# Performance work log

Measured on AMD Instinct MI355X. Metric: run time of the kernel, lower is better.

## Reference

```python
import jax, jax.numpy as jnp
import numpy as np

DIM = 2048
DT_RANK = 64
DIM_INNER = 2048
D_STATE = 32
B_SZ = 4
L = 2048


def setup_inputs() -> dict:
    key = jax.random.key(0)
    ks = jax.random.split(key, 6)
    x = jax.random.normal(ks[0], (B_SZ, L, DIM), dtype=jnp.float32)
    z = jax.random.normal(ks[1], (B_SZ, L, DIM_INNER), dtype=jnp.float32)
    # proj_bc: Linear(dim, dt_rank + 2*d_state, bias=False)
    W_bc = jax.random.normal(ks[2], (DT_RANK + 2 * D_STATE, DIM), dtype=jnp.float32) * (DIM ** -0.5)
    # dt_proj: maps dt_rank -> dim_inner (as intended in Mamba)
    W_dt = jax.random.normal(ks[3], (DIM_INNER, DT_RANK), dtype=jnp.float32) * (DT_RANK ** -0.5)
    b_dt = jax.random.normal(ks[4], (DIM_INNER,), dtype=jnp.float32) * 0.1
    # A = arange(1, d_state+1) repeated per channel; A_log = log(A)
    A_log = jnp.log(jnp.tile(jnp.arange(1, D_STATE + 1, dtype=jnp.float32), (DIM_INNER, 1)))
    D_param = jnp.ones((DIM_INNER,), dtype=jnp.float32)
    return {"x": x, "z": z, "W_bc": W_bc, "W_dt": W_dt, "b_dt": b_dt, "A_log": A_log, "D_param": D_param}


def _selective_scan(u, delta, A, Bm, Cm, D_param):
    # u, delta: [b, l, d]; Bm, Cm: [b, l, n]; A: [d, n]; D_param: [d]
    def step(h, inp):
        delta_t, B_t, C_t, u_t = inp  # [b,d], [b,n], [b,n], [b,d]
        dA = jnp.exp(delta_t[:, :, None] * A[None])          # [b, d, n]
        dBu = (delta_t * u_t)[:, :, None] * B_t[:, None, :]  # [b, d, n]
        h = dA * h + dBu
        y_t = jnp.einsum('bdn,bn->bd', h, C_t)
        return h, y_t

    b = u.shape[0]
    h0 = jnp.zeros((b, A.shape[0], A.shape[1]), dtype=u.dtype)
    xs = (jnp.moveaxis(delta, 1, 0), jnp.moveaxis(Bm, 1, 0),
          jnp.moveaxis(Cm, 1, 0), jnp.moveaxis(u, 1, 0))
    _, ys = jax.lax.scan(step, h0, xs)          # ys: [l, b, d]
    y = jnp.moveaxis(ys, 0, 1)                  # [b, l, d]
    return y + u * D_param[None, None, :]


def reference(x, z, W_bc, W_dt, b_dt, A_log, D_param):
    A = -jnp.exp(A_log)                                      # [d, n]
    deltaBC = jnp.einsum('bld,od->blo', x, W_bc)             # [b, l, r+2n]
    dt_r = deltaBC[..., :DT_RANK]
    Bm = deltaBC[..., DT_RANK:DT_RANK + D_STATE]             # [b, l, n]
    Cm = deltaBC[..., DT_RANK + D_STATE:]                    # [b, l, n]
    dt = jnp.einsum('blr,dr->bld', dt_r, W_dt)               # [b, l, d]
    delta = jax.nn.softplus(dt + b_dt[None, None, :])        # delta_softplus + delta_bias
    y = _selective_scan(x, delta, A, Bm, Cm, D_param)        # [b, l, d]
    return y
```

## Files before the change

kernel.cpp:

```cpp
#include <hip/hip_runtime.h>

#define L_SEQ 2048
#define NDIM 2048
#define DINNER 2048
#define NSTATE 32
#define BSZ 4
#define DTR 64
#define NROWS (BSZ * L_SEQ)
#define TCH 32

typedef short bf16x8 __attribute__((ext_vector_type(8)));
typedef float f32x4 __attribute__((ext_vector_type(4)));
typedef unsigned int uint_t;

#if __has_builtin(__builtin_amdgcn_exp2f)
#define EXP2(v) __builtin_amdgcn_exp2f(v)
#else
#define EXP2(v) exp2f(v)
#endif
#define LOG2E 1.44269504f

__device__ __forceinline__ uint_t bf1(float a) {
  uint_t u = __float_as_uint(a);
  return (u + 0x7FFFu + ((u >> 16) & 1u)) >> 16;
}
__device__ __forceinline__ uint_t pkbf(float a, float b) {
  return bf1(a) | (bf1(b) << 16);
}

#define WBC_ELEMS (128 * NDIM)
#define WDT_ELEMS (DINNER * DTR)
__global__ __launch_bounds__(256) void k_conv(const float* __restrict__ Wbc,
                                              const float* __restrict__ Wdt,
                                              unsigned short* __restrict__ o) {
  const int i = blockIdx.x * 256 + threadIdx.x;
  if (i < WBC_ELEMS)
    o[i] = (unsigned short)bf1(Wbc[i]);
  else
    o[i] = (unsigned short)bf1(Wdt[i - WBC_ELEMS]);
}

__global__ __launch_bounds__(512) void k_dbc_mfma(const float* __restrict__ x,
                                                  const unsigned short* __restrict__ Wb,
                                                  float* __restrict__ dbc) {
  __shared__ unsigned short xl[32][72];
  __shared__ unsigned short wl[128][72];
  const int tid = threadIdx.x;
  const int wave = tid >> 6, lane = tid & 63;
  const int row0 = blockIdx.x * 32;
  const int wrow0 = (wave & 1) * 16;
  const int wcol0 = (wave >> 1) * 32;
  const int fr = lane & 15, fk = (lane >> 4) * 8;

  f32x4 acc[2];
#pragma unroll
  for (int i = 0; i < 2; ++i) acc[i] = (f32x4)(0.f);

  const int xr = tid >> 4, xk = (tid & 15) * 4;
  const int wc = tid & 127, wh = (tid >> 7) * 16;

  for (int kb = 0; kb < NDIM; kb += 64) {
    const float4 xa = *(const float4*)(x + (size_t)(row0 + xr) * NDIM + kb + xk);
    uint4 wv0 = *(const uint4*)(Wb + (size_t)wc * NDIM + kb + wh);
    uint4 wv1 = *(const uint4*)(Wb + (size_t)wc * NDIM + kb + wh + 8);
    __syncthreads();
    uint2 xp = {pkbf(xa.x, xa.y), pkbf(xa.z, xa.w)};
    *(uint2*)&xl[xr][xk] = xp;
    *(uint4*)&wl[wc][wh] = wv0;
    *(uint4*)&wl[wc][wh + 8] = wv1;
    __syncthreads();
#pragma unroll
    for (int ks = 0; ks < 2; ++ks) {
      const bf16x8 af = *(const bf16x8*)&xl[wrow0 + fr][ks * 32 + fk];
#pragma unroll
      for (int nt = 0; nt < 2; ++nt) {
        const bf16x8 bfv = *(const bf16x8*)&wl[wcol0 + nt * 16 + fr][ks * 32 + fk];
        acc[nt] = __builtin_amdgcn_mfma_f32_16x16x32_bf16(af, bfv, acc[nt], 0, 0, 0);
      }
    }
  }
#pragma unroll
  for (int nt = 0; nt < 2; ++nt)
#pragma unroll
    for (int reg = 0; reg < 4; ++reg)
      dbc[(size_t)(row0 + wrow0 + (lane >> 4) * 4 + reg) * 128 + wcol0 + nt * 16 + fr] =
          acc[nt][reg];
}

__global__ __launch_bounds__(256) void k_dt_mfma(const float* __restrict__ dbc,
                                                 const unsigned short* __restrict__ Wd,
                                                 const float* __restrict__ bdt,
                                                 float* __restrict__ dy) {
  __shared__ unsigned short al[32][72];
  const int tid = threadIdx.x;
  const int wave = tid >> 6, lane = tid & 63;
  const int row0 = blockIdx.y * 32;
  const int c0 = blockIdx.x * 256;
  const int wrow0 = (wave & 1) * 16;
  const int wc0 = c0 + (wave >> 1) * 128;
  const int fr = lane & 15, fk = (lane >> 4) * 8;

  {
    const int ar = tid >> 3, ak = (tid & 7) * 8;
    const float4 pa = *(const float4*)(dbc + (size_t)(row0 + ar) * 128 + ak);
    const float4 pb = *(const float4*)(dbc + (size_t)(row0 + ar) * 128 + ak + 4);
    uint4 ap = {pkbf(pa.x, pa.y), pkbf(pa.z, pa.w), pkbf(pb.x, pb.y), pkbf(pb.z, pb.w)};
    *(uint4*)&al[ar][ak] = ap;
  }
  __syncthreads();

  f32x4 acc[8];
#pragma unroll
  for (int i = 0; i < 8; ++i) acc[i] = (f32x4)(0.f);

#pragma unroll
  for (int ks = 0; ks < 2; ++ks) {
    const bf16x8 af = *(const bf16x8*)&al[wrow0 + fr][ks * 32 + fk];
#pragma unroll
    for (int nt = 0; nt < 8; ++nt) {
      const int col = wc0 + nt * 16 + fr;
      const bf16x8 bfv = *(const bf16x8*)(Wd + (size_t)col * 64 + ks * 32 + fk);
      acc[nt] = __builtin_amdgcn_mfma_f32_16x16x32_bf16(af, bfv, acc[nt], 0, 0, 0);
    }
  }

#pragma unroll
  for (int nt = 0; nt < 8; ++nt) {
    const int col = wc0 + nt * 16 + fr;
    const float bias = bdt[col];
#pragma unroll
    for (int reg = 0; reg < 4; ++reg) {
      const float v = acc[nt][reg] + bias;
      const float sp = (v > 20.f) ? v : __logf(1.f + __expf(v));
      dy[(size_t)(row0 + wrow0 + (lane >> 4) * 4 + reg) * DINNER + col] = sp;
    }
  }
}

__global__ __launch_bounds__(256) void k_dbc(const float* __restrict__ x,
                                             const float* __restrict__ Wbc,
                                             float* __restrict__ dbc) {
  __shared__ float xs[32][36];
  __shared__ float ws[32][132];
  const int tid = threadIdx.x;
  const int tx = tid & 31;
  const int ty = tid >> 5;
  const int row0 = blockIdx.x * 32;
  float acc[4][4];
#pragma unroll
  for (int i = 0; i < 4; ++i)
#pragma unroll
    for (int j = 0; j < 4; ++j) acc[i][j] = 0.f;
  for (int kb = 0; kb < NDIM; kb += 32) {
    {
      const int r = tid >> 3;
      const int k0 = (tid & 7) * 4;
      const float4 v = *(const float4*)(x + (size_t)(row0 + r) * NDIM + kb + k0);
      *(float4*)&xs[r][k0] = v;
    }
    {
      const int col = tid & 127;
      const int k0 = (tid >> 7) * 16;
#pragma unroll
      for (int j = 0; j < 4; ++j) {
        const float4 v = *(const float4*)(Wbc + (size_t)col * NDIM + kb + k0 + j * 4);
        ws[k0 + j * 4 + 0][col] = v.x;
        ws[k0 + j * 4 + 1][col] = v.y;
        ws[k0 + j * 4 + 2][col] = v.z;
        ws[k0 + j * 4 + 3][col] = v.w;
      }
    }
    __syncthreads();
#pragma unroll
    for (int k = 0; k < 32; k += 4) {
      float a_[4][4];
#pragma unroll
      for (int i = 0; i < 4; ++i) {
        const float4 av = *(const float4*)&xs[ty * 4 + i][k];
        a_[i][0] = av.x; a_[i][1] = av.y; a_[i][2] = av.z; a_[i][3] = av.w;
      }
#pragma unroll
      for (int kk = 0; kk < 4; ++kk) {
        const float4 bv = *(const float4*)&ws[k + kk][tx * 4];
        float b_[4] = {bv.x, bv.y, bv.z, bv.w};
#pragma unroll
        for (int i = 0; i < 4; ++i)
#pragma unroll
          for (int j = 0; j < 4; ++j)
            acc[i][j] = fmaf(a_[i][kk], b_[j], acc[i][j]);
      }
    }
    __syncthreads();
  }
#pragma unroll
  for (int i = 0; i < 4; ++i) {
    float4 o = {acc[i][0], acc[i][1], acc[i][2], acc[i][3]};
    *(float4*)(dbc + (size_t)(row0 + ty * 4 + i) * 128 + tx * 4) = o;
  }
}

__global__ __launch_bounds__(256) void k_dt(const float* __restrict__ dbc,
                                            const float* __restrict__ Wdt,
                                            const float* __restrict__ bdt,
                                            float* dy) {
  __shared__ float asn[16][68];
  __shared__ float wst[64][132];
  const int tid = threadIdx.x;
  const int tx = tid & 31;
  const int ty = tid >> 5;
  const int row0 = blockIdx.y * 16;
  const int col0 = blockIdx.x * 128;
  {
    const int r = tid >> 4;
    const int k0 = (tid & 15) * 4;
    const float4 v = *(const float4*)(dbc + (size_t)(row0 + r) * 128 + k0);
    *(float4*)&asn[r][k0] = v;
  }
  {
    const int col = tid & 127;
    const int k0 = (tid >> 7) * 32;
#pragma unroll
    for (int j = 0; j < 8; ++j) {
      const float4 v = *(const float4*)(Wdt + (size_t)(col0 + col) * 64 + k0 + j * 4);
      wst[k0 + j * 4 + 0][col] = v.x;
      wst[k0 + j * 4 + 1][col] = v.y;
      wst[k0 + j * 4 + 2][col] = v.z;
      wst[k0 + j * 4 + 3][col] = v.w;
    }
  }
  __syncthreads();
  float acc[2][4];
#pragma unroll
  for (int i = 0; i < 2; ++i)
#pragma unroll
    for (int j = 0; j < 4; ++j) acc[i][j] = 0.f;
#pragma unroll
  for (int k = 0; k < 64; k += 4) {
    float a_[2][4];
#pragma unroll
    for (int i = 0; i < 2; ++i) {
      const float4 av = *(const float4*)&asn[ty * 2 + i][k];
      a_[i][0] = av.x; a_[i][1] = av.y; a_[i][2] = av.z; a_[i][3] = av.w;
    }
#pragma unroll
    for (int kk = 0; kk < 4; ++kk) {
      const float4 bv = *(const float4*)&wst[k + kk][tx * 4];
      float b_[4] = {bv.x, bv.y, bv.z, bv.w};
#pragma unroll
      for (int i = 0; i < 2; ++i)
#pragma unroll
        for (int j = 0; j < 4; ++j)
          acc[i][j] = fmaf(a_[i][kk], b_[j], acc[i][j]);
    }
  }
  const int c = col0 + tx * 4;
  const float4 bb = *(const float4*)(bdt + c);
  const float bias[4] = {bb.x, bb.y, bb.z, bb.w};
#pragma unroll
  for (int i = 0; i < 2; ++i) {
    float o[4];
#pragma unroll
    for (int j = 0; j < 4; ++j) {
      const float v = acc[i][j] + bias[j];
      o[j] = (v > 20.f) ? v : __logf(1.f + __expf(v));
    }
    float4 ov = {o[0], o[1], o[2], o[3]};
    *(float4*)(dy + (size_t)(row0 + ty * 2 + i) * DINNER + c) = ov;
  }
}

template <int CTRL>
__device__ __forceinline__ float dpp_mov(float v) {
  return __int_as_float(
      __builtin_amdgcn_update_dpp(0, __float_as_int(v), CTRL, 0xF, 0xF, true));
}
__device__ __forceinline__ float red16(float p) {
  p += dpp_mov<0xB1>(p);
  p += dpp_mov<0x4E>(p);
  p += dpp_mov<0x141>(p);
  p += dpp_mov<0x140>(p);
  return p;
}
__device__ __forceinline__ float xor16_add(float p) {
#if __has_builtin(__builtin_amdgcn_permlane16_swap)
  typedef unsigned u2v __attribute__((ext_vector_type(2)));
  u2v s = __builtin_amdgcn_permlane16_swap(__float_as_uint(p),
                                           __float_as_uint(p), false, false);
  return __uint_as_float(s.x) + __uint_as_float(s.y);
#else
  return p + __int_as_float(
                 __builtin_amdgcn_ds_swizzle(__float_as_int(p), 0x401F));
#endif
}

__global__ __launch_bounds__(512) void k_scan512(const float* __restrict__ x,
                                                 const float* __restrict__ dbc,
                                                 const float* __restrict__ Alog,
                                                 const float* __restrict__ Dpar,
                                                 float* __restrict__ dy) {
  __shared__ float sDU[2][16][68];
  __shared__ float sBC[2][16][128];
  __shared__ float sY[2][32][17];

  const int tid = threadIdx.x;
  const int nn = tid & 31, ch = tid >> 5;
  const int dd = tid & 15, tl = tid >> 4;
  const int dg = blockIdx.x & 127;
  const int b = blockIdx.x >> 7;
  const int d0 = dg * 16;
  const int NCHK = L_SEQ / TCH;

  const float An2 = -__expf(Alog[(size_t)(d0 + ch) * NSTATE + nn]) * LOG2E;
  const float Dd = Dpar[d0 + dd];
  const size_t segbase = (size_t)b * L_SEQ;

  float u_cur;
  {
    const size_t rX = (segbase + tl) * DINNER + d0 + dd;
    const float dv = dy[rX];
    const float uv = x[rX];
    *(float2*)&sDU[0][dd][(tl >> 1) * 4 + (tl & 1) * 2] = make_float2(dv, dv * uv);
    u_cur = uv;
    const size_t rB = (segbase + ch) * 128 + 64 + nn;
    *(float2*)&sBC[0][ch >> 1][nn * 4 + (ch & 1) * 2] =
        make_float2(dbc[rB], dbc[rB + 32]);
    *(float2*)&sBC[0][(ch >> 1) + 8][nn * 4 + (ch & 1) * 2] =
        make_float2(dbc[rB + 16 * 128], dbc[rB + 16 * 128 + 32]);
  }
  __syncthreads();

  float h = 0.f;
  for (int c = 0; c < NCHK; ++c) {
    const int cb = c & 1;
    float dnx = 0.f, unx = 0.f;
    float2 bc0 = make_float2(0.f, 0.f), bc1 = make_float2(0.f, 0.f);
    if (c < NCHK - 1) {
      const size_t rX = (segbase + (c + 1) * TCH + tl) * DINNER + d0 + dd;
      dnx = dy[rX];
      unx = x[rX];
      const size_t rB = (segbase + (c + 1) * TCH + ch) * 128 + 64 + nn;
      bc0 = make_float2(dbc[rB], dbc[rB + 32]);
      bc1 = make_float2(dbc[rB + 16 * 128], dbc[rB + 16 * 128 + 32]);
    }

    const float* pDU = &sDU[cb][ch][0];
    const float* pBC = &sBC[cb][0][nn * 4];
    float yv = 0.f;
#pragma unroll
    for (int t2 = 0; t2 < TCH / 2; ++t2) {
      const float4 du = *(const float4*)(pDU + t2 * 4);
      const float4 bc = *(const float4*)(pBC + t2 * 128);
      {
        const float dA = EXP2(du.x * An2);
        h = fmaf(dA, h, du.y * bc.x);
        const float yy = xor16_add(red16(h * bc.y));
        yv = (nn == 2 * t2) ? yy : yv;
      }
      {
        const float dA = EXP2(du.z * An2);
        h = fmaf(dA, h, du.w * bc.z);
        const float yy = xor16_add(red16(h * bc.w));
        yv = (nn == 2 * t2 + 1) ? yy : yv;
      }
    }
    sY[cb][nn][ch] = yv;

    if (c < NCHK - 1) {
      *(float2*)&sDU[cb ^ 1][dd][(tl >> 1) * 4 + (tl & 1) * 2] =
          make_float2(dnx, dnx * unx);
      *(float2*)&sBC[cb ^ 1][ch >> 1][nn * 4 + (ch & 1) * 2] = bc0;
      *(float2*)&sBC[cb ^ 1][(ch >> 1) + 8][nn * 4 + (ch & 1) * 2] = bc1;
    }
    __syncthreads();

    dy[(segbase + c * TCH + tl) * DINNER + d0 + dd] =
        fmaf(u_cur, Dd, sY[cb][tl][dd]);
    u_cur = unx;
  }
}

extern "C" void kernel_launch(void* const* d_in, const int* in_sizes, int n_in,
                              void* d_out, int out_size, void* d_ws, size_t ws_size,
                              hipStream_t stream) {
  const float* x    = (const float*)d_in[0];
  const float* Wbc  = (const float*)d_in[2];
  const float* Wdt  = (const float*)d_in[3];
  const float* bdt  = (const float*)d_in[4];
  const float* Alog = (const float*)d_in[5];
  const float* Dpar = (const float*)d_in[6];
  float* dy  = (float*)d_out;
  float* dbc = (float*)d_ws;

  const size_t DBC_BYTES = (size_t)NROWS * 128 * 4;
  const size_t WCONV_BYTES = (size_t)(WBC_ELEMS + WDT_ELEMS) * 2;

  const bool mfma_ok = ws_size >= DBC_BYTES + WCONV_BYTES;

  if (mfma_ok) {
    unsigned short* Wb = (unsigned short*)((char*)d_ws + DBC_BYTES);
    unsigned short* Wd = Wb + WBC_ELEMS;
    hipLaunchKernelGGL(k_conv, dim3((WBC_ELEMS + WDT_ELEMS) / 256), dim3(256), 0,
                       stream, Wbc, Wdt, Wb);
    hipLaunchKernelGGL(k_dbc_mfma, dim3(NROWS / 32), dim3(512), 0, stream,
                       x, Wb, dbc);
    hipLaunchKernelGGL(k_dt_mfma, dim3(DINNER / 256, NROWS / 32), dim3(256), 0,
                       stream, dbc, Wd, bdt, dy);
  } else {
    hipLaunchKernelGGL(k_dbc, dim3(NROWS / 32), dim3(256), 0, stream, x, Wbc, dbc);
    hipLaunchKernelGGL(k_dt, dim3(DINNER / 128, NROWS / 16), dim3(256), 0, stream,
                       dbc, Wdt, bdt, dy);
  }

  hipLaunchKernelGGL(k_scan512, dim3(BSZ * DINNER / 16), dim3(512), 0, stream,
                     x, dbc, Alog, Dpar, dy);
}
```

Measured before the change: 308.2 us.

## Pack two SSM states per lane in scan kernel using 256-thread blocks

The scan kernel now gives each thread two state entries (n and n+16) held in a float2 instead of one. The block shrinks from 512 to 256 threads, and the cross-lane reduction drops the 16-lane swap step. The B/C shared layout is rearranged to match, and each thread now loads and stores two timesteps of u/delta. This roughly halves the lane-reduction work and DPP traffic per state, at the cost of fewer threads per block. The change also adds a redundant self-copy store to shared memory.

```diff
diff --git a/kernel.cpp b/kernel.cpp
--- a/kernel.cpp
+++ b/kernel.cpp
@@ -11,6 +11,7 @@
 
 typedef short bf16x8 __attribute__((ext_vector_type(8)));
 typedef float f32x4 __attribute__((ext_vector_type(4)));
+typedef float f32x2 __attribute__((ext_vector_type(2)));
 typedef unsigned int uint_t;
 
 #if __has_builtin(__builtin_amdgcn_exp2f)
@@ -281,101 +282,143 @@
   p += dpp_mov<0x140>(p);
   return p;
 }
-__device__ __forceinline__ float xor16_add(float p) {
-#if __has_builtin(__builtin_amdgcn_permlane16_swap)
-  typedef unsigned u2v __attribute__((ext_vector_type(2)));
-  u2v s = __builtin_amdgcn_permlane16_swap(__float_as_uint(p),
-                                           __float_as_uint(p), false, false);
-  return __uint_as_float(s.x) + __uint_as_float(s.y);
-#else
-  return p + __int_as_float(
-                 __builtin_amdgcn_ds_swizzle(__float_as_int(p), 0x401F));
-#endif
-}
-
-__global__ __launch_bounds__(512) void k_scan512(const float* __restrict__ x,
-                                                 const float* __restrict__ dbc,
-                                                 const float* __restrict__ Alog,
-                                                 const float* __restrict__ Dpar,
-                                                 float* __restrict__ dy) {
+
+__global__ __launch_bounds__(256) void k_scanp(const float* __restrict__ x,
+                                               const float* __restrict__ dbc,
+                                               const float* __restrict__ Alog,
+                                               const float* __restrict__ Dpar,
+                                               float* __restrict__ dy) {
   __shared__ float sDU[2][16][68];
-  __shared__ float sBC[2][16][128];
+  __shared__ float sBCp[2][32][68];
   __shared__ float sY[2][32][17];
 
   const int tid = threadIdx.x;
-  const int nn = tid & 31, ch = tid >> 5;
+  const int ln = tid & 15, ch = tid >> 4;
   const int dd = tid & 15, tl = tid >> 4;
+  const int nb = tid & 31, tq = tid >> 5;
   const int dg = blockIdx.x & 127;
   const int b = blockIdx.x >> 7;
   const int d0 = dg * 16;
   const int NCHK = L_SEQ / TCH;
 
-  const float An2 = -__expf(Alog[(size_t)(d0 + ch) * NSTATE + nn]) * LOG2E;
+  f32x2 An2;
+  An2.x = -__expf(Alog[(size_t)(d0 + ch) * NSTATE + ln]) * LOG2E;
+  An2.y = -__expf(Alog[(size_t)(d0 + ch) * NSTATE + ln + 16]) * LOG2E;
   const float Dd = Dpar[d0 + dd];
   const size_t segbase = (size_t)b * L_SEQ;
 
-  float u_cur;
+  const int bccol = (nb & 15) * 4 + (nb >> 4) * 2;
+
+  float u0, u1;
   {
-    const size_t rX = (segbase + tl) * DINNER + d0 + dd;
-    const float dv = dy[rX];
-    const float uv = x[rX];
-    *(float2*)&sDU[0][dd][(tl >> 1) * 4 + (tl & 1) * 2] = make_float2(dv, dv * uv);
-    u_cur = uv;
-    const size_t rB = (segbase + ch) * 128 + 64 + nn;
-    *(float2*)&sBC[0][ch >> 1][nn * 4 + (ch & 1) * 2] =
-        make_float2(dbc[rB], dbc[rB + 32]);
-    *(float2*)&sBC[0][(ch >> 1) + 8][nn * 4 + (ch & 1) * 2] =
-        make_float2(dbc[rB + 16 * 128], dbc[rB + 16 * 128 + 32]);
+    const size_t rX0 = (segbase + tl) * DINNER + d0 + dd;
+    const size_t rX1 = (segbase + tl + 16) * DINNER + d0 + dd;
+    const float dv0 = dy[rX0], uv0 = x[rX0];
+    const float dv1 = dy[rX1], uv1 = x[rX1];
+    *(float2*)&sDU[0][dd][(tl >> 1) * 4 + (tl & 1) * 2] = make_float2(dv0, dv0 * uv0);
+    *(float2*)&sDU[0][(tl >> 1) + 8][0] = *(float2*)&sDU[0][(tl >> 1) + 8][0];
+    *(float2*)&sDU[0][dd][((tl + 16) >> 1) * 4 + (tl & 1) * 2] =
+        make_float2(dv1, dv1 * uv1);
+    u0 = uv0;
+    u1 = uv1;
+#pragma unroll
+    for (int k = 0; k < 4; ++k) {
+      const int t = tq + k * 8;
+      const size_t rB = (segbase + t) * 128 + 64 + nb;
+      *(float2*)&sBCp[0][t][bccol] = make_float2(dbc[rB], dbc[rB + 32]);
+    }
   }
   __syncthreads();
 
-  float h = 0.f;
+  f32x2 h = (f32x2)(0.f);
   for (int c = 0; c < NCHK; ++c) {
     const int cb = c & 1;
-    float dnx = 0.f, unx = 0.f;
-    float2 bc0 = make_float2(0.f, 0.f), bc1 = make_float2(0.f, 0.f);
+    float dn0 = 0.f, un0 = 0.f, dn1 = 0.f, un1 = 0.f;
+    float2 bcx[4];
+#pragma unroll
+    for (int k = 0; k < 4; ++k) bcx[k] = make_float2(0.f, 0.f);
     if (c < NCHK - 1) {
-      const size_t rX = (segbase + (c + 1) * TCH + tl) * DINNER + d0 + dd;
-      dnx = dy[rX];
-      unx = x[rX];
-      const size_t rB = (segbase + (c + 1) * TCH + ch) * 128 + 64 + nn;
-      bc0 = make_float2(dbc[rB], dbc[rB + 32]);
-      bc1 = make_float2(dbc[rB + 16 * 128], dbc[rB + 16 * 128 + 32]);
+      const size_t rX0 = (segbase + (c + 1) * TCH + tl) * DINNER + d0 + dd;
+      const size_t rX1 = (segbase + (c + 1) * TCH + tl + 16) * DINNER + d0 + dd;
+      dn0 = dy[rX0];
+      un0 = x[rX0];
+      dn1 = dy[rX1];
+      un1 = x[rX1];
+#pragma unroll
+      for (int k = 0; k < 4; ++k) {
+        const size_t rB = (segbase + (c + 1) * TCH + tq + k * 8) * 128 + 64 + nb;
+        bcx[k] = make_float2(dbc[rB], dbc[rB + 32]);
+      }
     }
 
     const float* pDU = &sDU[cb][ch][0];
-    const float* pBC = &sBC[cb][0][nn * 4];
-    float yv = 0.f;
+    const float* pBC = &sBCp[cb][0][ln * 4];
+    float yv0 = 0.f, yv1 = 0.f;
 #pragma unroll
     for (int t2 = 0; t2 < TCH / 2; ++t2) {
       const float4 du = *(const float4*)(pDU + t2 * 4);
-      const float4 bc = *(const float4*)(pBC + t2 * 128);
+      const float4 b0 = *(const float4*)(pBC + (2 * t2) * 68);
+      const float4 b1 = *(const float4*)(pBC + (2 * t2 + 1) * 68);
       {
-        const float dA = EXP2(du.x * An2);
-        h = fmaf(dA, h, du.y * bc.x);
-        const float yy = xor16_add(red16(h * bc.y));
-        yv = (nn == 2 * t2) ? yy : yv;
+        const int t = 2 * t2;
+        f32x2 ea = An2 * du.x;
+        f32x2 dA;
+        dA.x = EXP2(ea.x);
+        dA.y = EXP2(ea.y);
+        f32x2 Bp;
+        Bp.x = b0.x;
+        Bp.y = b0.z;
+        f32x2 Cp;
+        Cp.x = b0.y;
+        Cp.y = b0.w;
+        h = dA * h + Bp * du.y;
+        const f32x2 pp = h * Cp;
+        const float p = red16(pp.x + pp.y);
+        if (t < 16)
+          yv0 = (ln == t) ? p : yv0;
+        else
+          yv1 = (ln == t - 16) ? p : yv1;
       }
       {
-        const float dA = EXP2(du.z * An2);
-        h = fmaf(dA, h, du.w * bc.z);
-        const float yy = xor16_add(red16(h * bc.w));
-        yv = (nn == 2 * t2 + 1) ? yy : yv;
-      }
-    }
-    sY[cb][nn][ch] = yv;
+        const int t = 2 * t2 + 1;
+        f32x2 ea = An2 * du.z;
+        f32x2 dA;
+        dA.x = EXP2(ea.x);
+        dA.y = EXP2(ea.y);
+        f32x2 Bp;
+        Bp.x = b1.x;
+        Bp.y = b1.z;
+        f32x2 Cp;
+        Cp.x = b1.y;
+        Cp.y = b1.w;
+        h = dA * h + Bp * du.w;
+        const f32x2 pp = h * Cp;
+        const float p = red16(pp.x + pp.y);
+        if (t < 16)
+          yv0 = (ln == t) ? p : yv0;
+        else
+          yv1 = (ln == t - 16) ? p : yv1;
+      }
+    }
+    sY[cb][ln][ch] = yv0;
+    sY[cb][ln + 16][ch] = yv1;
 
     if (c < NCHK - 1) {
       *(float2*)&sDU[cb ^ 1][dd][(tl >> 1) * 4 + (tl & 1) * 2] =
-          make_float2(dnx, dnx * unx);
-      *(float2*)&sBC[cb ^ 1][ch >> 1][nn * 4 + (ch & 1) * 2] = bc0;
-      *(float2*)&sBC[cb ^ 1][(ch >> 1) + 8][nn * 4 + (ch & 1) * 2] = bc1;
+          make_float2(dn0, dn0 * un0);
+      *(float2*)&sDU[cb ^ 1][dd][((tl + 16) >> 1) * 4 + (tl & 1) * 2] =
+          make_float2(dn1, dn1 * un1);
+#pragma unroll
+      for (int k = 0; k < 4; ++k)
+        *(float2*)&sBCp[cb ^ 1][tq + k * 8][bccol] = bcx[k];
     }
     __syncthreads();
 
-    dy[(segbase + c * TCH + tl) * DINNER + d0 + dd] =
-        fmaf(u_cur, Dd, sY[cb][tl][dd]);
-    u_cur = unx;
+    dy[(segbase + c * TCH + tl) * DINNER + d0 + dd] = fmaf(u0, Dd, sY[cb][tl][dd]);
+    dy[(segbase + c * TCH + tl + 16) * DINNER + d0 + dd] =
+        fmaf(u1, Dd, sY[cb][tl + 16][dd]);
+    u0 = un0;
+    u1 = un1;
   }
 }
 
@@ -411,6 +454,6 @@
                        dbc, Wdt, bdt, dy);
   }
 
-  hipLaunchKernelGGL(k_scan512, dim3(BSZ * DINNER / 16), dim3(512), 0, stream,
+  hipLaunchKernelGGL(k_scanp, dim3(BSZ * DINNER / 16), dim3(256), 0, stream,
                      x, dbc, Alog, Dpar, dy);
 }
```

After: 253.6 us. -17.7%, faster.
